# Performance work log

Measured on AMD Instinct MI355X. Metric: run time of the kernel, lower is better.

## Reference

```python
import jax, jax.numpy as jnp
import numpy as np

POOLED_SIZES = [12, 16, 20, 24]
NUM_HEADS = 8
EPS_LN = 1e-5


def _pool_mat(in_size, out_size):
    # torch adaptive_avg_pool1d/2d semantics as an averaging matrix [out, in]
    m = np.zeros((out_size, in_size), np.float32)
    for i in range(out_size):
        s = (i * in_size) // out_size
        e = -((-(i + 1) * in_size) // out_size)  # ceil
        m[i, s:e] = 1.0 / (e - s)
    return jnp.asarray(m)


def _dwconv(x, w, b):
    # depthwise 3x3, stride 1, padding 1 (NCHW, OIHW with I=1)
    y = jax.lax.conv_general_dilated(
        x, w, (1, 1), 'SAME', feature_group_count=x.shape[1],
        dimension_numbers=('NCHW', 'OIHW', 'NCHW'))
    return y + b[None, :, None, None]


def _ln(x, g, b):
    m = x.mean(-1, keepdims=True)
    v = jnp.mean((x - m) ** 2, axis=-1, keepdims=True)
    return (x - m) / jnp.sqrt(v + EPS_LN) * g + b


def setup_inputs() -> dict:
    key = jax.random.key(0)
    ks = jax.random.split(key, 16)
    B, H, W, C = 4, 56, 56, 256
    hid = 4 * C
    nrm = lambda k, shape, s=0.02: jax.random.normal(k, shape, jnp.float32) * s
    inp = {
        'x': jax.random.normal(ks[0], (B, H * W, C), jnp.float32),
        'cpe_w': nrm(ks[1], (C, 1, 3, 3)), 'cpe_b': jnp.zeros((C,), jnp.float32),
        'norm1_w': jnp.ones((C,), jnp.float32), 'norm1_b': jnp.zeros((C,), jnp.float32),
        'q_w': nrm(ks[2], (C, C)),
        'kv_w': nrm(ks[3], (2 * C, C)),
        'attn_norm_w': jnp.ones((C,), jnp.float32), 'attn_norm_b': jnp.zeros((C,), jnp.float32),
        'proj_w': nrm(ks[4], (C, C)), 'proj_b': jnp.zeros((C,), jnp.float32),
        'norm2_w': jnp.ones((C,), jnp.float32), 'norm2_b': jnp.zeros((C,), jnp.float32),
        'fc1_w': nrm(ks[5], (hid, C)), 'fc1_b': jnp.zeros((hid,), jnp.float32),
        'irb_conv_w': nrm(ks[6], (hid, 1, 3, 3)), 'irb_conv_b': jnp.zeros((hid,), jnp.float32),
        'fc2_w': nrm(ks[7], (C, hid)), 'fc2_b': jnp.zeros((C,), jnp.float32),
        'H': H, 'W': W,
    }
    for i in range(4):
        inp[f'dconv{i}_w'] = nrm(ks[8 + i], (C, 1, 3, 3))
        inp[f'dconv{i}_b'] = jnp.zeros((C,), jnp.float32)
    return inp


def _forward(x, cpe_w, cpe_b, norm1_w, norm1_b, q_w, kv_w, attn_norm_w, attn_norm_b,
             proj_w, proj_b, dconv0_w, dconv0_b, dconv1_w, dconv1_b, dconv2_w, dconv2_b,
             dconv3_w, dconv3_b, norm2_w, norm2_b, fc1_w, fc1_b, irb_conv_w, irb_conv_b,
             fc2_w, fc2_b, H, W):
    B, N, C = x.shape
    nh = NUM_HEADS
    hd = C // nh
    scale = hd ** -0.5
    # conditional positional encoding: x = cpe(x) + x
    xi = x.transpose(0, 2, 1).reshape(B, C, H, W)
    xi = _dwconv(xi, cpe_w, cpe_b) + xi
    x = xi.reshape(B, C, N).transpose(0, 2, 1)
    # ---- pyramid pooling attention ----
    xn = _ln(x, norm1_w, norm1_b)
    q = (xn @ q_w.T).reshape(B, N, nh, hd).transpose(0, 2, 1, 3)  # [B,nh,N,hd]
    x_ = xn.transpose(0, 2, 1).reshape(B, C, H, W)
    dws = [(dconv0_w, dconv0_b), (dconv1_w, dconv1_b),
           (dconv2_w, dconv2_b), (dconv3_w, dconv3_b)]
    pools = []
    for p, (dw, db) in zip(POOLED_SIZES, dws):
        ph = _pool_mat(H, p)
        pw = _pool_mat(W, p)
        pool = jnp.einsum('oi,bcij,pj->bcop', ph, x_, pw)  # adaptive avg pool (p,p)
        pool = pool + _dwconv(pool, dw, db)
        pools.append(pool.reshape(B, C, -1))
    pools = jnp.concatenate(pools, axis=2).transpose(0, 2, 1)  # [B,P,C], P=1376
    pools = _ln(pools, attn_norm_w, attn_norm_b)
    kv = (pools @ kv_w.T).reshape(B, -1, 2, nh, hd).transpose(2, 0, 3, 1, 4)
    k, v = kv[0], kv[1]  # [B,nh,P,hd]
    attn = jax.nn.softmax(jnp.einsum('bhnd,bhpd->bhnp', q, k) * scale, axis=-1)
    out = jnp.einsum('bhnp,bhpd->bhnd', attn, v).transpose(0, 2, 1, 3).reshape(B, N, C)
    out = out @ proj_w.T + proj_b
    x = x + out
    # ---- IRB FFN ----
    xn = _ln(x, norm2_w, norm2_b)
    xi = xn.transpose(0, 2, 1).reshape(B, C, H, W)
    h = jnp.einsum('oc,bchw->bohw', fc1_w, xi) + fc1_b[None, :, None, None]
    h = jax.nn.gelu(h, approximate=False)
    h = h + _dwconv(h, irb_conv_w, irb_conv_b)
    o = jnp.einsum('oc,bchw->bohw', fc2_w, h) + fc2_b[None, :, None, None]
    x = x + o.reshape(B, C, N).transpose(0, 2, 1)
    return x


def reference(x, cpe_w, cpe_b, norm1_w, norm1_b, q_w, kv_w, attn_norm_w, attn_norm_b,
              proj_w, proj_b, dconv0_w, dconv0_b, dconv1_w, dconv1_b, dconv2_w, dconv2_b,
              dconv3_w, dconv3_b, norm2_w, norm2_b, fc1_w, fc1_b, irb_conv_w, irb_conv_b,
              fc2_w, fc2_b, H, W):
    return _forward(x, cpe_w, cpe_b, norm1_w, norm1_b, q_w, kv_w, attn_norm_w, attn_norm_b,
                    proj_w, proj_b, dconv0_w, dconv0_b, dconv1_w, dconv1_b, dconv2_w, dconv2_b,
                    dconv3_w, dconv3_b, norm2_w, norm2_b, fc1_w, fc1_b, irb_conv_w, irb_conv_b,
                    fc2_w, fc2_b, H, W)
```

## Files before the change

kernel.cpp:

```cpp
#include <hip/hip_runtime.h>
#include <hip/hip_bf16.h>

#define BQ 4
#define HH 56
#define WW 56
#define NN (HH*WW)
#define CC 256
#define NHEAD 8
#define HD 32
#define PP 1376
#define PPAD 1408
#define HIDN 1024
#define EPS_LN 1e-5f
#define QSCALE_LOG2E 0.25503484f

typedef unsigned short bf16u;
typedef __attribute__((ext_vector_type(8))) short short8;
typedef __attribute__((ext_vector_type(4))) float f32x4;

__device__ __forceinline__ float bf2f(bf16u u){
  union { unsigned int i; float f; } v; v.i = ((unsigned int)u) << 16; return v.f;
}
__device__ __forceinline__ bf16u f2bf(float f){
  unsigned int x = __float_as_uint(f);
  x += 0x7fffu + ((x >> 16) & 1u);
  return (bf16u)(x >> 16);
}
__device__ __forceinline__ bf16u f2bf_r(float f){
  return (bf16u)((__float_as_uint(f) + 0x8000u) >> 16);
}
__device__ __forceinline__ void cvt4(const ushort4 u, float* d){
  d[0]=bf2f(u.x); d[1]=bf2f(u.y); d[2]=bf2f(u.z); d[3]=bf2f(u.w);
}

__global__ void k_init(const float* __restrict__ qw, const float* __restrict__ kvw,
                       const float* __restrict__ pw, const float* __restrict__ f1,
                       const float* __restrict__ f2, bf16u* __restrict__ wo,
                       const float* __restrict__ x, const float* __restrict__ w,
                       const float* __restrict__ bias, const float* __restrict__ g,
                       const float* __restrict__ be, float* __restrict__ x1,
                       bf16u* __restrict__ xnb){
  if (blockIdx.x < 768){
    int off = (blockIdx.x*256 + threadIdx.x) * 4;
    const float* s;
    if (off < 65536)       s = qw  + off;
    else if (off < 196608) s = kvw + off - 65536;
    else if (off < 262144) s = pw  + off - 196608;
    else if (off < 524288) s = f1  + off - 262144;
    else                   s = f2  + off - 524288;
    float4 v = *(const float4*)s;
    ushort4 u = {f2bf(v.x), f2bf(v.y), f2bf(v.z), f2bf(v.w)};
    *(ushort4*)(wo + off) = u;
    return;
  }
  int t = threadIdx.x;
  int pix = (blockIdx.x - 768)*4 + (t >> 6);
  int b = pix / NN, n = pix % NN;
  int hy = n / WW, wx = n % WW;
  int c0 = (t & 63) * 4;
  float wv[4][9];
  float acc[4];
#pragma unroll
  for (int cc = 0; cc < 4; cc++){
    acc[cc] = bias[c0+cc];
#pragma unroll
    for (int k = 0; k < 9; k++) wv[cc][k] = w[(c0+cc)*9 + k];
  }
  const float* xb = x + (size_t)b*NN*CC + c0;
#pragma unroll
  for (int kh = 0; kh < 3; kh++){
    int iy = hy + kh - 1;
    if (iy < 0 || iy >= HH) continue;
#pragma unroll
    for (int kw = 0; kw < 3; kw++){
      int ix = wx + kw - 1;
      if (ix < 0 || ix >= WW) continue;
      float4 v = *(const float4*)&xb[(size_t)(iy*WW+ix)*CC];
      int k = kh*3+kw;
      acc[0] += v.x*wv[0][k]; acc[1] += v.y*wv[1][k];
      acc[2] += v.z*wv[2][k]; acc[3] += v.w*wv[3][k];
    }
  }
  float4 cv = *(const float4*)&xb[(size_t)n*CC];
  float o0 = cv.x + acc[0], o1 = cv.y + acc[1];
  float o2 = cv.z + acc[2], o3 = cv.w + acc[3];
  float4 ov = {o0,o1,o2,o3};
  *(float4*)&x1[(size_t)pix*CC + c0] = ov;
  float s  = o0+o1+o2+o3;
  float s2 = o0*o0+o1*o1+o2*o2+o3*o3;
#pragma unroll
  for (int off = 32; off; off >>= 1){
    s  += __shfl_xor(s,  off);
    s2 += __shfl_xor(s2, off);
  }
  float mean = s * (1.f/CC);
  float var  = s2 * (1.f/CC) - mean*mean;
  float rstd = rsqrtf(var + EPS_LN);
  float4 gv = *(const float4*)&g[c0];
  float4 bv = *(const float4*)&be[c0];
  float y0 = (o0-mean)*rstd*gv.x + bv.x;
  float y1 = (o1-mean)*rstd*gv.y + bv.y;
  float y2 = (o2-mean)*rstd*gv.z + bv.z;
  float y3 = (o3-mean)*rstd*gv.w + bv.w;
  ushort4 yb = {f2bf_r(y0), f2bf_r(y1), f2bf_r(y2), f2bf_r(y3)};
  *(ushort4*)&xnb[(size_t)pix*CC + c0] = yb;
}

__global__ void k_ln_bf16(const float* __restrict__ X, const float* __restrict__ g,
                          const float* __restrict__ be, bf16u* __restrict__ Y){
  int row = blockIdx.x;
  int t = threadIdx.x;
  float v = X[(size_t)row*CC + t];
  float s = v, s2 = v*v;
#pragma unroll
  for (int off = 32; off; off >>= 1){
    s  += __shfl_down(s,  off);
    s2 += __shfl_down(s2, off);
  }
  __shared__ float red[10];
  int wv_ = t >> 6, ln = t & 63;
  if (ln == 0){ red[wv_] = s; red[4+wv_] = s2; }
  __syncthreads();
  if (t == 0){
    float S  = red[0]+red[1]+red[2]+red[3];
    float S2 = red[4]+red[5]+red[6]+red[7];
    float mean = S * (1.f/CC);
    float var  = S2 * (1.f/CC) - mean*mean;
    red[8] = mean; red[9] = rsqrtf(var + EPS_LN);
  }
  __syncthreads();
  float mean = red[8], rstd = red[9];
  Y[(size_t)row*CC + t] = f2bf_r((v - mean) * rstd * g[t] + be[t]);
}

__global__ void k_pool(const bf16u* __restrict__ xnb, float* __restrict__ praw){
  int bp = blockIdx.x;
  int b = bp / PP, p = bp % PP;
  int ps, pi;
  if (p < 144)      { ps = 12; pi = p; }
  else if (p < 400) { ps = 16; pi = p - 144; }
  else if (p < 800) { ps = 20; pi = p - 400; }
  else              { ps = 24; pi = p - 800; }
  int oi = pi / ps, oj = pi % ps;
  int si = oi*HH/ps, ei = ((oi+1)*HH + ps - 1)/ps;
  int sj = oj*WW/ps, ej = ((oj+1)*WW + ps - 1)/ps;
  int c = threadIdx.x;
  const bf16u* xb = xnb + (size_t)b*NN*CC + c;
  float acc = 0.f;
  for (int i = si; i < ei; i++)
    for (int j = sj; j < ej; j++)
      acc += bf2f(xb[(size_t)(i*WW+j)*CC]);
  praw[(size_t)bp*CC + c] = acc / (float)((ei-si)*(ej-sj));
}

__global__ void k_pooldw_ln(const float* __restrict__ praw,
    const float* w0, const float* b0, const float* w1, const float* b1,
    const float* w2, const float* b2, const float* w3, const float* b3,
    const float* __restrict__ g, const float* __restrict__ be,
    bf16u* __restrict__ pools){
  int bp = blockIdx.x;
  int b = bp / PP, p = bp % PP;
  int ps, pi, off; const float *w, *bi;
  if (p < 144)      { ps=12; pi=p;     off=0;   w=w0; bi=b0; }
  else if (p < 400) { ps=16; pi=p-144; off=144; w=w1; bi=b1; }
  else if (p < 800) { ps=20; pi=p-400; off=400; w=w2; bi=b2; }
  else              { ps=24; pi=p-800; off=800; w=w3; bi=b3; }
  int oi = pi/ps, oj = pi%ps;
  int c = threadIdx.x;
  const float* base = praw + (size_t)(b*PP + off)*CC + c;
  float acc = bi[c];
#pragma unroll
  for (int kh = 0; kh < 3; kh++){
    int ii = oi + kh - 1; if (ii < 0 || ii >= ps) continue;
#pragma unroll
    for (int kw = 0; kw < 3; kw++){
      int jj = oj + kw - 1; if (jj < 0 || jj >= ps) continue;
      acc += base[(size_t)(ii*ps+jj)*CC] * w[c*9 + kh*3 + kw];
    }
  }
  float v = base[(size_t)(oi*ps+oj)*CC] + acc;
  float s = v, s2 = v*v;
#pragma unroll
  for (int o2_ = 32; o2_; o2_ >>= 1){
    s  += __shfl_down(s,  o2_);
    s2 += __shfl_down(s2, o2_);
  }
  __shared__ float red[10];
  int wv_ = c >> 6, ln = c & 63;
  if (ln == 0){ red[wv_] = s; red[4+wv_] = s2; }
  __syncthreads();
  if (c == 0){
    float S  = red[0]+red[1]+red[2]+red[3];
    float S2 = red[4]+red[5]+red[6]+red[7];
    float mean = S * (1.f/CC);
    float var  = S2 * (1.f/CC) - mean*mean;
    red[8] = mean; red[9] = rsqrtf(var + EPS_LN);
  }
  __syncthreads();
  float mean = red[8], rstd = red[9];
  pools[(size_t)bp*CC + c] = f2bf_r((v - mean) * rstd * g[c] + be[c]);
}

#define GST 40
template<int NT, bool OUT_BF16, bool HAS_BIAS, bool DO_GELU, bool HAS_RES, bool VT_OUT>
__global__ __launch_bounds__(256) void k_gemm_mfma(const bf16u* __restrict__ A,
                       const bf16u* __restrict__ Wt,
                       const float* __restrict__ bias, void* Outp,
                       const float* Res, bf16u* __restrict__ vtout,
                       int M, int Nout, int K, float oscale){
  constexpr int NW = (NT == 128) ? 4 : 2;
  __shared__ bf16u Ash[128*GST];
  __shared__ bf16u Bsh[NT*GST];
  int t = threadIdx.x;
  int wave = t >> 6, lane = t & 63, quad = lane >> 4, l16 = lane & 15;
  int m0 = blockIdx.y * 128, n0 = blockIdx.x * NT;
  int wm = (wave >> 1) * 64;
  int wn = (wave & 1) * (NT/2);
  int srow = t >> 1, scol = (t & 1) * 16;
  f32x4 zero = {0.f,0.f,0.f,0.f};
  f32x4 acc[4][NW];
#pragma unroll
  for (int i = 0; i < 4; i++)
#pragma unroll
    for (int j = 0; j < NW; j++) acc[i][j] = zero;
  for (int k0 = 0; k0 < K; k0 += 32){
    __syncthreads();
    {
      const bf16u* ap = A + (size_t)(m0+srow)*K + k0 + scol;
      uint4 u = *(const uint4*)ap;
      uint4 v = *(const uint4*)(ap+8);
      *(uint4*)&Ash[srow*GST + scol]     = u;
      *(uint4*)&Ash[srow*GST + scol + 8] = v;
    }
    if constexpr (NT == 128){
      const bf16u* bp = Wt + (size_t)(n0+srow)*K + k0 + scol;
      uint4 u = *(const uint4*)bp;
      uint4 v = *(const uint4*)(bp+8);
      *(uint4*)&Bsh[srow*GST + scol]     = u;
      *(uint4*)&Bsh[srow*GST + scol + 8] = v;
    } else {
      int br = t >> 2, bc = (t & 3) * 8;
      const bf16u* bp = Wt + (size_t)(n0+br)*K + k0 + bc;
      uint4 u = *(const uint4*)bp;
      *(uint4*)&Bsh[br*GST + bc] = u;
    }
    __syncthreads();
    short8 af[4], bfr[NW];
#pragma unroll
    for (int mi = 0; mi < 4; mi++)
      af[mi] = *(const short8*)&Ash[(wm + mi*16 + l16)*GST + quad*8];
#pragma unroll
    for (int ni = 0; ni < NW; ni++)
      bfr[ni] = *(const short8*)&Bsh[(wn + ni*16 + l16)*GST + quad*8];
#pragma unroll
    for (int mi = 0; mi < 4; mi++)
#pragma unroll
      for (int ni = 0; ni < NW; ni++)
        acc[mi][ni] = __builtin_amdgcn_mfma_f32_16x16x32_bf16(af[mi], bfr[ni], acc[mi][ni], 0,0,0);
  }
#pragma unroll
  for (int mi = 0; mi < 4; mi++){
#pragma unroll
    for (int r = 0; r < 4; r++){
      int row = m0 + wm + mi*16 + quad*4 + r;
#pragma unroll
      for (int ni = 0; ni < NW; ni++){
        int col = n0 + wn + ni*16 + l16;
        float v = acc[mi][ni][r] * oscale;
        if constexpr (HAS_BIAS) v += bias[col];
        if constexpr (DO_GELU)  v = 0.5f*v*(1.f + erff(v*0.70710678118654752f));
        if constexpr (HAS_RES)  v += Res[(size_t)row*Nout + col];
        if constexpr (VT_OUT){
          if (col < CC){
            ((bf16u*)Outp)[(size_t)row*Nout + col] = f2bf_r(v);
          } else {
            int bb = row / PP, pp = row - bb*PP;
            vtout[((size_t)(bb*CC + (col - CC)))*PPAD + pp] = f2bf_r(v);
          }
        } else if constexpr (OUT_BF16){
          ((bf16u*)Outp)[(size_t)row*Nout + col] = f2bf_r(v);
        } else {
          ((float*)Outp)[(size_t)row*Nout + col] = v;
        }
      }
    }
  }
}

#define KST 40
#define VST 72
__global__ __launch_bounds__(256) void k_attn_mfma(const bf16u* __restrict__ q,
                       const bf16u* __restrict__ kvb, const bf16u* __restrict__ vt,
                       bf16u* __restrict__ out){
  __shared__ bf16u Ksh[2][64*KST];
  __shared__ bf16u Vsh[2][32*VST];
  int t = threadIdx.x;
  int wave = t >> 6, lane = t & 63, quad = lane >> 4, l16 = lane & 15;
  int bid = blockIdx.x;
  int qt = bid % (NN/64);
  int h  = (bid / (NN/64)) % NHEAD;
  int b  = bid / ((NN/64)*NHEAD);
  int q0 = qt*64 + wave*16;
  const bf16u* qptr = q + (size_t)(b*NN + q0 + l16)*CC + h*HD + quad*8;
  short8 qf = *(const short8*)qptr;
  f32x4 zero = {0.f,0.f,0.f,0.f};
  f32x4 o0 = zero, o1 = zero;
  float ls = 0.f;
  int ksr = t >> 2, ksc = (t & 3) * 8;
  int vsr = t >> 3, vsc = (t & 7) * 8;
  const bf16u* ksrc = kvb + (size_t)(b*PP + ksr)*(2*CC) + h*HD + ksc;
  const bf16u* vsrc = vt  + (size_t)(b*CC + h*HD + vsr)*PPAD + vsc;
  int kstore = ksr*KST + ksc;
  int vstore = vsr*VST + vsc;
  int g0 = ((l16 & 12) << 1) | (l16 & 3);
  int koffA = g0 * KST + quad*8;
  int koffB = koffA + 4*KST;
  int voff0 = l16*VST + quad*8;
  int voff1 = (16 + l16)*VST + quad*8;

  uint4 kreg = *(const uint4*)ksrc;
  uint4 vreg = *(const uint4*)vsrc;
  *(uint4*)&Ksh[0][kstore] = kreg;
  *(uint4*)&Vsh[0][vstore] = vreg;
  ksrc += (size_t)64*(2*CC); vsrc += 64;
  kreg = *(const uint4*)ksrc; vreg = *(const uint4*)vsrc;
  __syncthreads();

#define PAIR(KB, VB, cb) { \
    short8 kfa = *(const short8*)&KB[cb*KST + koffA]; \
    short8 kfb = *(const short8*)&KB[cb*KST + koffB]; \
    f32x4 sa = __builtin_amdgcn_mfma_f32_16x16x32_bf16(kfa, qf, zero, 0,0,0); \
    f32x4 sb = __builtin_amdgcn_mfma_f32_16x16x32_bf16(kfb, qf, zero, 0,0,0); \
    float ea0 = __builtin_amdgcn_exp2f(sa[0]), ea1 = __builtin_amdgcn_exp2f(sa[1]); \
    float ea2 = __builtin_amdgcn_exp2f(sa[2]), ea3 = __builtin_amdgcn_exp2f(sa[3]); \
    float eb0 = __builtin_amdgcn_exp2f(sb[0]), eb1 = __builtin_amdgcn_exp2f(sb[1]); \
    float eb2 = __builtin_amdgcn_exp2f(sb[2]), eb3 = __builtin_amdgcn_exp2f(sb[3]); \
    ls += ((ea0+ea1)+(ea2+ea3)) + ((eb0+eb1)+(eb2+eb3)); \
    short8 pa; \
    pa[0]=(short)f2bf_r(ea0); pa[1]=(short)f2bf_r(ea1); \
    pa[2]=(short)f2bf_r(ea2); pa[3]=(short)f2bf_r(ea3); \
    pa[4]=(short)f2bf_r(eb0); pa[5]=(short)f2bf_r(eb1); \
    pa[6]=(short)f2bf_r(eb2); pa[7]=(short)f2bf_r(eb3); \
    short8 vf0 = *(const short8*)&VB[cb + voff0]; \
    short8 vf1 = *(const short8*)&VB[cb + voff1]; \
    o0 = __builtin_amdgcn_mfma_f32_16x16x32_bf16(pa, vf0, o0, 0,0,0); \
    o1 = __builtin_amdgcn_mfma_f32_16x16x32_bf16(pa, vf1, o1, 0,0,0); }

  for (int ch = 0; ch < PPAD/64 - 1; ch++){
    int cur = ch & 1;
    bf16u* KB = &Ksh[cur][0];
    bf16u* VB = &Vsh[cur][0];
    *(uint4*)&Ksh[cur^1][kstore] = kreg;
    *(uint4*)&Vsh[cur^1][vstore] = vreg;
    if (ch < PPAD/64 - 2){
      ksrc += (size_t)64*(2*CC); vsrc += 64;
      kreg = *(const uint4*)ksrc; vreg = *(const uint4*)vsrc;
    }
    PAIR(KB, VB, 0)
    PAIR(KB, VB, 32)
    __syncthreads();
  }
  {
    bf16u* KB = &Ksh[1][0];
    bf16u* VB = &Vsh[1][0];
    PAIR(KB, VB, 0)
  }
#undef PAIR

  ls += __shfl_xor(ls, 16); ls += __shfl_xor(ls, 32);
#pragma unroll
  for (int r = 0; r < 4; r++){
    int qq = quad*4 + r;
    float inv = 1.f / __shfl(ls, qq);
    size_t base = (size_t)(b*NN + q0 + qq)*CC + h*HD;
    out[base + l16]      = f2bf_r(o0[r]*inv);
    out[base + 16 + l16] = f2bf_r(o1[r]*inv);
  }
}

#define DWSEG 8
__global__ __launch_bounds__(256) void k_dwh(const bf16u* __restrict__ h, const float* __restrict__ w,
                      const float* __restrict__ bias, bf16u* __restrict__ h2){
  const int nseg = WW/DWSEG;
  int bid = blockIdx.x;
  int xseg = bid % nseg;
  int y    = (bid / nseg) % HH;
  int b    = bid / (nseg*HH);
  int t = threadIdx.x;
  int c0 = t*4;
  int x0 = xseg*DWSEG;
  float wv[36];
  {
    const float4* wp = (const float4*)(w + (size_t)c0*9);
#pragma unroll
    for (int i = 0; i < 9; i++){
      float4 v = wp[i];
      wv[i*4+0]=v.x; wv[i*4+1]=v.y; wv[i*4+2]=v.z; wv[i*4+3]=v.w;
    }
  }
  float4 bi4 = *(const float4*)&bias[c0];
  float bi[4] = {bi4.x, bi4.y, bi4.z, bi4.w};
  const bf16u* rowc = h + ((size_t)b*NN + (size_t)y*WW)*HIDN + c0;
  const bf16u* rowm = (y > 0)    ? rowc - (size_t)WW*HIDN : rowc;
  const bf16u* rowp = (y < HH-1) ? rowc + (size_t)WW*HIDN : rowc;
  if (y == 0){
#pragma unroll
    for (int cc = 0; cc < 4; cc++){ wv[cc*9+0]=0.f; wv[cc*9+1]=0.f; wv[cc*9+2]=0.f; }
  }
  if (y == HH-1){
#pragma unroll
    for (int cc = 0; cc < 4; cc++){ wv[cc*9+6]=0.f; wv[cc*9+7]=0.f; wv[cc*9+8]=0.f; }
  }
  float win[3][3][4];
  ushort4 rawA[3], rawB[3];
  if (x0 == 0){
#pragma unroll
    for (int r = 0; r < 3; r++)
#pragma unroll
      for (int cc = 0; cc < 4; cc++) win[0][r][cc] = 0.f;
  } else {
    size_t o = (size_t)(x0-1)*HIDN;
    ushort4 a0 = *(const ushort4*)&rowm[o];
    ushort4 a1 = *(const ushort4*)&rowc[o];
    ushort4 a2 = *(const ushort4*)&rowp[o];
    cvt4(a0, win[0][0]); cvt4(a1, win[0][1]); cvt4(a2, win[0][2]);
  }
  {
    size_t o = (size_t)x0*HIDN;
    ushort4 a0 = *(const ushort4*)&rowm[o];
    ushort4 a1 = *(const ushort4*)&rowc[o];
    ushort4 a2 = *(const ushort4*)&rowp[o];
    cvt4(a0, win[1][0]); cvt4(a1, win[1][1]); cvt4(a2, win[1][2]);
  }
  {
    size_t o = (size_t)(x0+1)*HIDN;
    rawA[0] = *(const ushort4*)&rowm[o];
    rawA[1] = *(const ushort4*)&rowc[o];
    rawA[2] = *(const ushort4*)&rowp[o];
  }
#pragma unroll
  for (int x = 0; x < DWSEG; x++){
    ushort4* cur = (x & 1) ? rawB : rawA;
    ushort4* nxt = (x & 1) ? rawA : rawB;
    if (x < DWSEG-1){
      int xg = x0 + x + 2;
      if (xg < WW){
        size_t o = (size_t)xg*HIDN;
        nxt[0] = *(const ushort4*)&rowm[o];
        nxt[1] = *(const ushort4*)&rowc[o];
        nxt[2] = *(const ushort4*)&rowp[o];
      } else {
        ushort4 z = {0,0,0,0};
        nxt[0] = z; nxt[1] = z; nxt[2] = z;
      }
    }
    int s2 = (x+2)%3, sm = x%3, sc_ = (x+1)%3;
    cvt4(cur[0], win[s2][0]); cvt4(cur[1], win[s2][1]); cvt4(cur[2], win[s2][2]);
    float o0[4];
#pragma unroll
    for (int cc = 0; cc < 4; cc++){
      float a = bi[cc];
      a += win[sm][0][cc]*wv[cc*9+0] + win[sc_][0][cc]*wv[cc*9+1] + win[s2][0][cc]*wv[cc*9+2];
      a += win[sm][1][cc]*wv[cc*9+3] + win[sc_][1][cc]*wv[cc*9+4] + win[s2][1][cc]*wv[cc*9+5];
      a += win[sm][2][cc]*wv[cc*9+6] + win[sc_][2][cc]*wv[cc*9+7] + win[s2][2][cc]*wv[cc*9+8];
      o0[cc] = win[sc_][1][cc] + a;
    }
    ushort4 ou = {f2bf_r(o0[0]), f2bf_r(o0[1]), f2bf_r(o0[2]), f2bf_r(o0[3])};
    *(ushort4*)&h2[((size_t)b*NN + (size_t)y*WW + x0 + x)*HIDN + c0] = ou;
  }
}

extern "C" void kernel_launch(void* const* d_in, const int* in_sizes, int n_in,
                              void* d_out, int out_size, void* d_ws, size_t ws_size,
                              hipStream_t stream){
  const float* x      = (const float*)d_in[0];
  const float* cpe_w  = (const float*)d_in[1];
  const float* cpe_b  = (const float*)d_in[2];
  const float* n1w    = (const float*)d_in[3];
  const float* n1b    = (const float*)d_in[4];
  const float* q_w    = (const float*)d_in[5];
  const float* kv_w   = (const float*)d_in[6];
  const float* anw    = (const float*)d_in[7];
  const float* anb    = (const float*)d_in[8];
  const float* proj_w = (const float*)d_in[9];
  const float* proj_b = (const float*)d_in[10];
  const float* n2w    = (const float*)d_in[11];
  const float* n2b    = (const float*)d_in[12];
  const float* fc1_w  = (const float*)d_in[13];
  const float* fc1_b  = (const float*)d_in[14];
  const float* irb_w  = (const float*)d_in[15];
  const float* irb_b  = (const float*)d_in[16];
  const float* fc2_w  = (const float*)d_in[17];
  const float* fc2_b  = (const float*)d_in[18];
  const float* dw0    = (const float*)d_in[21];
  const float* db0    = (const float*)d_in[22];
  const float* dw1    = (const float*)d_in[23];
  const float* db1    = (const float*)d_in[24];
  const float* dw2    = (const float*)d_in[25];
  const float* db2    = (const float*)d_in[26];
  const float* dw3    = (const float*)d_in[27];
  const float* db3    = (const float*)d_in[28];

  const size_t BNC = (size_t)BQ*NN*CC;
  const size_t BPC = (size_t)BQ*PP*CC;
  const size_t BNH = (size_t)BQ*NN*HIDN;

  float* x1   = (float*)d_ws;
  bf16u* xnb  = (bf16u*)(x1 + BNC);
  bf16u* wbuf = xnb + BNC;
  bf16u* wq   = wbuf;
  bf16u* wkv  = wbuf + 65536;
  bf16u* wpj  = wbuf + 196608;
  bf16u* wf1  = wbuf + 262144;
  bf16u* wf2  = wbuf + 524288;
  float* A0   = (float*)(wbuf + 786432);
  bf16u* qb   = (bf16u*)A0;
  float* praw = (float*)(qb + BNC);
  bf16u* poolsb = (bf16u*)(praw + BPC);
  bf16u* kvb  = poolsb + BPC;
  bf16u* vtb  = kvb + (size_t)BQ*PP*2*CC;
  bf16u* hbuf = (bf16u*)A0;
  bf16u* h2buf = hbuf + BNH;

  k_init<<<768 + BQ*NN/4, 256, 0, stream>>>(q_w, kv_w, proj_w, fc1_w, fc2_w, wbuf,
                                            x, cpe_w, cpe_b, n1w, n1b, x1, xnb);
  k_gemm_mfma<64,true,false,false,false,false><<<dim3(CC/64, BQ*NN/128), 256, 0, stream>>>(
      xnb, wq, nullptr, qb, nullptr, nullptr, BQ*NN, CC, CC, QSCALE_LOG2E);
  k_pool<<<BQ*PP, 256, 0, stream>>>(xnb, praw);
  k_pooldw_ln<<<BQ*PP, 256, 0, stream>>>(praw, dw0,db0, dw1,db1, dw2,db2, dw3,db3,
                                         anw, anb, poolsb);
  k_gemm_mfma<64,true,false,false,false,true><<<dim3(2*CC/64, BQ*PP/128), 256, 0, stream>>>(
      poolsb, wkv, nullptr, kvb, nullptr, vtb, BQ*PP, 2*CC, CC, 1.0f);
  k_attn_mfma<<<BQ*NHEAD*(NN/64), 256, 0, stream>>>(qb, kvb, vtb, qb);
  k_gemm_mfma<64,false,true,false,true,false><<<dim3(CC/64, BQ*NN/128), 256, 0, stream>>>(
      qb, wpj, proj_b, x1, x1, nullptr, BQ*NN, CC, CC, 1.0f);
  k_ln_bf16<<<BQ*NN, 256, 0, stream>>>(x1, n2w, n2b, xnb);
  k_gemm_mfma<128,true,true,true,false,false><<<dim3(HIDN/128, BQ*NN/128), 256, 0, stream>>>(
      xnb, wf1, fc1_b, hbuf, nullptr, nullptr, BQ*NN, HIDN, CC, 1.0f);
  k_dwh<<<BQ*HH*(WW/DWSEG), 256, 0, stream>>>(hbuf, irb_w, irb_b, h2buf);
  k_gemm_mfma<64,false,true,false,true,false><<<dim3(CC/64, BQ*NN/128), 256, 0, stream>>>(
      h2buf, wf2, fc2_b, d_out, x1, nullptr, BQ*NN, CC, HIDN, 1.0f);
}
```

Measured before the change: 333.6 us.

## Double-buffer LDS tiles and prefetch global loads in MFMA GEMM

Converts the bf16 MFMA GEMM main loop to a double-buffered LDS scheme. The next K-slice is prefetched into registers and stored to the alternate buffer while the current one is consumed, so only one barrier per iteration remains. This is meant to hide global-load latency behind the MFMA work. In exchange it doubles the shared memory footprint and raises register pressure, which may lower occupancy.

Result: faster. 321.3 us (-3.7%).

```diff
diff --git a/kernel.cpp b/kernel.cpp
--- a/kernel.cpp
+++ b/kernel.cpp
@@ -209,54 +209,69 @@
                        const float* Res, bf16u* __restrict__ vtout,
                        int M, int Nout, int K, float oscale){
   constexpr int NW = (NT == 128) ? 4 : 2;
-  __shared__ bf16u Ash[128*GST];
-  __shared__ bf16u Bsh[NT*GST];
+  __shared__ bf16u Ash[2][128*GST];
+  __shared__ bf16u Bsh[2][NT*GST];
   int t = threadIdx.x;
   int wave = t >> 6, lane = t & 63, quad = lane >> 4, l16 = lane & 15;
   int m0 = blockIdx.y * 128, n0 = blockIdx.x * NT;
   int wm = (wave >> 1) * 64;
   int wn = (wave & 1) * (NT/2);
   int srow = t >> 1, scol = (t & 1) * 16;
+  int br = (NT == 128) ? srow : (t >> 2);
+  int bc = (NT == 128) ? scol : ((t & 3) * 8);
+  int astore = srow*GST + scol;
+  int bstore = br*GST + bc;
+  const bf16u* ap = A  + (size_t)(m0+srow)*K + scol;
+  const bf16u* bp = Wt + (size_t)(n0+br)*K + bc;
+
+  uint4 a0 = *(const uint4*)ap, a1 = *(const uint4*)(ap+8);
+  uint4 b0 = *(const uint4*)bp, b1;
+  if constexpr (NT == 128) b1 = *(const uint4*)(bp+8);
+  *(uint4*)&Ash[0][astore]     = a0;
+  *(uint4*)&Ash[0][astore + 8] = a1;
+  *(uint4*)&Bsh[0][bstore] = b0;
+  if constexpr (NT == 128) *(uint4*)&Bsh[0][bstore + 8] = b1;
+  ap += 32; bp += 32;
+  a0 = *(const uint4*)ap; a1 = *(const uint4*)(ap+8);
+  b0 = *(const uint4*)bp;
+  if constexpr (NT == 128) b1 = *(const uint4*)(bp+8);
+  __syncthreads();
+
   f32x4 zero = {0.f,0.f,0.f,0.f};
   f32x4 acc[4][NW];
 #pragma unroll
   for (int i = 0; i < 4; i++)
 #pragma unroll
     for (int j = 0; j < NW; j++) acc[i][j] = zero;
-  for (int k0 = 0; k0 < K; k0 += 32){
-    __syncthreads();
-    {
-      const bf16u* ap = A + (size_t)(m0+srow)*K + k0 + scol;
-      uint4 u = *(const uint4*)ap;
-      uint4 v = *(const uint4*)(ap+8);
-      *(uint4*)&Ash[srow*GST + scol]     = u;
-      *(uint4*)&Ash[srow*GST + scol + 8] = v;
-    }
-    if constexpr (NT == 128){
-      const bf16u* bp = Wt + (size_t)(n0+srow)*K + k0 + scol;
-      uint4 u = *(const uint4*)bp;
-      uint4 v = *(const uint4*)(bp+8);
-      *(uint4*)&Bsh[srow*GST + scol]     = u;
-      *(uint4*)&Bsh[srow*GST + scol + 8] = v;
-    } else {
-      int br = t >> 2, bc = (t & 3) * 8;
-      const bf16u* bp = Wt + (size_t)(n0+br)*K + k0 + bc;
-      uint4 u = *(const uint4*)bp;
-      *(uint4*)&Bsh[br*GST + bc] = u;
-    }
-    __syncthreads();
+
+  int nks = K >> 5;
+  for (int ks = 0; ks < nks; ks++){
+    int cur = ks & 1;
+    if (ks < nks-1){
+      *(uint4*)&Ash[cur^1][astore]     = a0;
+      *(uint4*)&Ash[cur^1][astore + 8] = a1;
+      *(uint4*)&Bsh[cur^1][bstore] = b0;
+      if constexpr (NT == 128) *(uint4*)&Bsh[cur^1][bstore + 8] = b1;
+      if (ks < nks-2){
+        ap += 32; bp += 32;
+        a0 = *(const uint4*)ap; a1 = *(const uint4*)(ap+8);
+        b0 = *(const uint4*)bp;
+        if constexpr (NT == 128) b1 = *(const uint4*)(bp+8);
+      }
+    }
     short8 af[4], bfr[NW];
 #pragma unroll
     for (int mi = 0; mi < 4; mi++)
-      af[mi] = *(const short8*)&Ash[(wm + mi*16 + l16)*GST + quad*8];
+      af[mi] = *(const short8*)&Ash[cur][(wm + mi*16 + l16)*GST + quad*8];
 #pragma unroll
     for (int ni = 0; ni < NW; ni++)
-      bfr[ni] = *(const short8*)&Bsh[(wn + ni*16 + l16)*GST + quad*8];
+      bfr[ni] = *(const short8*)&Bsh[cur][(wn + ni*16 + l16)*GST + quad*8];
 #pragma unroll
     for (int mi = 0; mi < 4; mi++)
 #pragma unroll
       for (int ni = 0; ni < NW; ni++)
         acc[mi][ni] = __builtin_amdgcn_mfma_f32_16x16x32_bf16(af[mi], bfr[ni], acc[mi][ni], 0,0,0);
+    if (ks < nks-1) __syncthreads();
   }
 #pragma unroll
   for (int mi = 0; mi < 4; mi++){
```
